# Optimization experiments

Measured on AMD Instinct MI355X. Metric: run time of the kernel, lower is better.

## Reference

```python
import jax, jax.numpy as jnp
import numpy as np

NUM_USERS = 100000
NUM_ITEMS = 50000
N_NODES = NUM_USERS + NUM_ITEMS
LATENT_DIM = 64
SBERT_DIM = 384
NUM_LAYERS = 3
N_EDGES = 2_000_000


def setup_inputs() -> dict:
    key = jax.random.key(0)
    k1, k2, k3, k4 = jax.random.split(key, 4)
    edge_index = jax.random.randint(k1, (2, N_EDGES), 0, N_NODES, dtype=jnp.int32)
    user_emb = jax.random.normal(k2, (NUM_USERS, LATENT_DIM), dtype=jnp.float32) * 0.1
    book_bert = jax.random.normal(k3, (NUM_ITEMS, SBERT_DIM), dtype=jnp.float32)
    # torch Linear weight layout: [out_features, in_features]
    w_proj = jax.random.normal(k4, (LATENT_DIM, SBERT_DIM), dtype=jnp.float32) * (1.0 / np.sqrt(SBERT_DIM))
    return {"edge_index": edge_index, "user_emb": user_emb, "book_bert": book_bert, "w_proj": w_proj}


def reference(edge_index, user_emb, book_bert, w_proj):
    src, dst = edge_index[0], edge_index[1]
    # initial embeddings: [users ; proj(book_bert)] -> [N, D]
    book_emb = book_bert @ w_proj.T
    emb0 = jnp.concatenate([user_emb, book_emb], axis=0)

    # symmetric gcn_norm without self-loops (PyG LGConv default)
    ones = jnp.ones((src.shape[0],), dtype=emb0.dtype)
    deg = jax.ops.segment_sum(ones, dst, num_segments=N_NODES)
    dis = jnp.where(deg > 0, jax.lax.rsqrt(jnp.maximum(deg, 1.0)), 0.0)
    norm = dis[src] * dis[dst]  # [E]

    x = emb0
    acc = emb0
    for _ in range(NUM_LAYERS):
        # out[dst] += norm * x[src]  (gather-scatter SpMM)
        msgs = norm[:, None] * x[src]  # [E, D]
        x = jax.ops.segment_sum(msgs, dst, num_segments=N_NODES)
        acc = acc + x
    out = acc / jnp.asarray(NUM_LAYERS + 1, dtype=emb0.dtype)
    return (emb0, out)
```

## Files before the change

kernel.cpp:

```cpp
#include <hip/hip_runtime.h>
#include <hip/hip_bf16.h>
#include <stdint.h>

#define NUM_USERS 100000
#define NUM_ITEMS 50000
#define N_NODES   150000
#define LATENT    64
#define SBERT     384
#define N_EDGES   2000000
#define OUT_OFF   (N_NODES * LATENT)
#define NBUCK     586
#define BCAP      4096
#define EPB       4096

typedef __hip_bfloat16 bf16;

__device__ __forceinline__ int ufl(int v) { return __builtin_amdgcn_readfirstlane(v); }

__global__ void k_zero_bcnt(int* __restrict__ bcnt) {
    int i = blockIdx.x * 256 + threadIdx.x;
    if (i < NBUCK) bcnt[i] = 0;
}

__global__ __launch_bounds__(256) void k_bin(const int* __restrict__ src,
                                             const int* __restrict__ dst,
                                             int* __restrict__ bcnt,
                                             unsigned* __restrict__ bin) {
    __shared__ int hist[NBUCK];
    __shared__ int base[NBUCK];
    const int tid = threadIdx.x;
    for (int i = tid; i < NBUCK; i += 256) hist[i] = 0;
    const int e0 = blockIdx.x * EPB;

    unsigned rec[16];
    int bb[16];
#pragma unroll
    for (int j = 0; j < 16; ++j) {
        int e = e0 + tid + j * 256;
        if (e < N_EDGES) {
            int d = __builtin_nontemporal_load(dst + e);
            int s = __builtin_nontemporal_load(src + e);
            bb[j]  = d >> 8;
            rec[j] = (unsigned)s | ((unsigned)(d & 255) << 18);
        } else {
            bb[j] = -1;
        }
    }
    __syncthreads();
#pragma unroll
    for (int j = 0; j < 16; ++j)
        if (bb[j] >= 0) atomicAdd(&hist[bb[j]], 1);
    __syncthreads();
    for (int i = tid; i < NBUCK; i += 256) {
        int c = hist[i];
        base[i] = c ? atomicAdd(&bcnt[i], c) : 0;
        hist[i] = 0;
    }
    __syncthreads();
    int p[16];
#pragma unroll
    for (int j = 0; j < 16; ++j)
        if (bb[j] >= 0) p[j] = atomicAdd(&hist[bb[j]], 1);
#pragma unroll
    for (int j = 0; j < 16; ++j)
        if (bb[j] >= 0)
            bin[(size_t)bb[j] * BCAP + base[bb[j]] + p[j]] = rec[j];
}

__global__ __launch_bounds__(1024) void k_bscan(const int* __restrict__ bcnt,
                                                int* __restrict__ bbase) {
    __shared__ int sm[1024];
    int tid = threadIdx.x;
    int v = (tid < NBUCK) ? bcnt[tid] : 0;
    sm[tid] = v;
    __syncthreads();
    for (int off = 1; off < 1024; off <<= 1) {
        int t = (tid >= off) ? sm[tid - off] : 0;
        __syncthreads();
        sm[tid] += t;
        __syncthreads();
    }
    if (tid <= NBUCK) bbase[tid] = (tid == 0) ? 0 : sm[tid - 1];
}

__global__ __launch_bounds__(256) void k_build(const unsigned* __restrict__ bin,
                                               const int* __restrict__ bcnt,
                                               const int* __restrict__ bbase,
                                               int* __restrict__ rp,
                                               float* __restrict__ dis,
                                               int* __restrict__ cws) {
    __shared__ int h[256];
    __shared__ int lc[256];
    const int tid   = threadIdx.x;
    const int b     = blockIdx.x;
    const int nbase = b << 8;
    const unsigned* mybin = bin + (size_t)b * BCAP;
    h[tid] = 0;
    __syncthreads();
    const int cnt  = bcnt[b];
    const int base = bbase[b];
    for (int i = tid; i < cnt; i += 256)
        atomicAdd(&h[__builtin_nontemporal_load(mybin + i) >> 18], 1);
    __syncthreads();
    int v = h[tid];
    __shared__ int sm[256];
    sm[tid] = v;
    __syncthreads();
    for (int off = 1; off < 256; off <<= 1) {
        int t = (tid >= off) ? sm[tid - off] : 0;
        __syncthreads();
        sm[tid] += t;
        __syncthreads();
    }
    int excl = sm[tid] - v;
    int n = nbase + tid;
    if (n < N_NODES) {
        rp[n]  = base + excl;
        dis[n] = (v > 0) ? rsqrtf((float)v) : 0.0f;
    }
    lc[tid] = base + excl;
    if (b == NBUCK - 1 && tid == 0) rp[N_NODES] = N_EDGES;
    __syncthreads();
    for (int i = tid; i < cnt; i += 256) {
        unsigned rec = __builtin_nontemporal_load(mybin + i);
        int dl = rec >> 18;
        int pos = atomicAdd(&lc[dl], 1);
        cws[pos] = (int)(rec & 0x3FFFF);
    }
}

__global__ void k_copy_user(const float* __restrict__ u, const float* __restrict__ dis,
                            float* __restrict__ out, bf16* __restrict__ y) {
    int i = blockIdx.x * 256 + threadIdx.x;
    if (i < NUM_USERS * LATENT) {
        float v = __builtin_nontemporal_load(u + i);
        out[i] = v;
        out[OUT_OFF + i] = v;
        float d = dis[i >> 6];
        y[i] = __float2bfloat16(d * v);
    }
}

__global__ __launch_bounds__(256) void k_proj(const float* __restrict__ bert,
                                              const float* __restrict__ w,
                                              const float* __restrict__ dis,
                                              float* __restrict__ out,
                                              bf16* __restrict__ y) {
    __shared__ float sB[128][33];
    __shared__ float sW[32][64];
    const int tid  = threadIdx.x;
    const int rb   = blockIdx.x * 128;
    const int col8 = (tid & 7) * 8;
    const int rowg = (tid >> 3) * 4;

    float acc[4][8];
#pragma unroll
    for (int i = 0; i < 4; ++i)
#pragma unroll
        for (int j = 0; j < 8; ++j) acc[i][j] = 0.0f;

    for (int kb = 0; kb < SBERT; kb += 32) {
        __syncthreads();
#pragma unroll
        for (int j = 0; j < 4; ++j) {
            int idx = tid + j * 256;
            int r  = idx >> 3;
            int k4 = (idx & 7) * 4;
            int rr = min(rb + r, NUM_ITEMS - 1);
            const float* bp = bert + (size_t)rr * SBERT + kb + k4;
            float4 v = make_float4(__builtin_nontemporal_load(bp + 0),
                                   __builtin_nontemporal_load(bp + 1),
                                   __builtin_nontemporal_load(bp + 2),
                                   __builtin_nontemporal_load(bp + 3));
            sB[r][k4 + 0] = v.x; sB[r][k4 + 1] = v.y;
            sB[r][k4 + 2] = v.z; sB[r][k4 + 3] = v.w;
        }
#pragma unroll
        for (int j = 0; j < 2; ++j) {
            int idx = tid + j * 256;
            int c  = idx >> 3;
            int k4 = (idx & 7) * 4;
            float4 v = *(const float4*)(w + (size_t)c * SBERT + kb + k4);
            sW[k4 + 0][c] = v.x; sW[k4 + 1][c] = v.y;
            sW[k4 + 2][c] = v.z; sW[k4 + 3][c] = v.w;
        }
        __syncthreads();
#pragma unroll
        for (int kk = 0; kk < 32; ++kk) {
            float4 w0 = *(const float4*)&sW[kk][col8];
            float4 w1 = *(const float4*)&sW[kk][col8 + 4];
#pragma unroll
            for (int i = 0; i < 4; ++i) {
                float a = sB[rowg + i][kk];
                acc[i][0] = fmaf(a, w0.x, acc[i][0]);
                acc[i][1] = fmaf(a, w0.y, acc[i][1]);
                acc[i][2] = fmaf(a, w0.z, acc[i][2]);
                acc[i][3] = fmaf(a, w0.w, acc[i][3]);
                acc[i][4] = fmaf(a, w1.x, acc[i][4]);
                acc[i][5] = fmaf(a, w1.y, acc[i][5]);
                acc[i][6] = fmaf(a, w1.z, acc[i][6]);
                acc[i][7] = fmaf(a, w1.w, acc[i][7]);
            }
        }
    }
#pragma unroll
    for (int i = 0; i < 4; ++i) {
        int r = rb + rowg + i;
        if (r < NUM_ITEMS) {
            int n = NUM_USERS + r;
            size_t o = (size_t)n * LATENT + col8;
            float d = dis[n];
            float4 f0 = make_float4(acc[i][0], acc[i][1], acc[i][2], acc[i][3]);
            float4 f1 = make_float4(acc[i][4], acc[i][5], acc[i][6], acc[i][7]);
            *(float4*)(out + o)           = f0;
            *(float4*)(out + o + 4)       = f1;
            *(float4*)(out + OUT_OFF + o) = f0;
            *(float4*)(out + OUT_OFF + o + 4) = f1;
#pragma unroll
            for (int j = 0; j < 8; ++j) y[o + j] = __float2bfloat16(d * acc[i][j]);
        }
    }
}

template <bool FINAL>
__global__ __launch_bounds__(256) void k_spmm(const bf16* __restrict__ y,
                                              const int* __restrict__ rp,
                                              const int* __restrict__ cws,
                                              const float* __restrict__ dis,
                                              bf16* __restrict__ yn,
                                              float* __restrict__ acc) {
    int lane = threadIdx.x & 63;
    int node = ufl(blockIdx.x * 4 + (threadIdx.x >> 6));
    int beg = rp[node];
    int end = rp[node + 1];
    int last = end - 1;
    float d = dis[node];
    size_t o = (size_t)node * LATENT + lane;
    float accv = acc[o];
    float a = 0.0f;
    for (int base = beg; base < end; base += 16) {
        int idx[16];
#pragma unroll
        for (int j = 0; j < 16; ++j)
            idx[j] = cws[min(base + j, last)];
        float v[16];
#pragma unroll
        for (int j = 0; j < 16; ++j)
            v[j] = __bfloat162float(y[(size_t)idx[j] * LATENT + lane]);
#pragma unroll
        for (int j = 0; j < 16; ++j)
            if (base + j <= last) a += v[j];
    }
    if (!FINAL) yn[o] = __float2bfloat16(d * d * a);
    float t = accv + d * a;
    acc[o] = FINAL ? t * 0.25f : t;
}

extern "C" void kernel_launch(void* const* d_in, const int* in_sizes, int n_in,
                              void* d_out, int out_size, void* d_ws, size_t ws_size,
                              hipStream_t stream) {
    const int*   ei    = (const int*)d_in[0];
    const float* uemb  = (const float*)d_in[1];
    const float* bert  = (const float*)d_in[2];
    const float* wproj = (const float*)d_in[3];
    float* out = (float*)d_out;

    char* ws = (char*)d_ws;
    size_t off = 0;
    auto carve = [&](size_t bytes) -> void* {
        void* p = ws + off;
        off += (bytes + 255) & ~(size_t)255;
        return p;
    };
    float*    dis    = (float*)carve(sizeof(float) * N_NODES);
    int*      rp     = (int*)carve(sizeof(int) * (N_NODES + 1));
    int*      bcnt   = (int*)carve(sizeof(int) * NBUCK);
    int*      bbase  = (int*)carve(sizeof(int) * (NBUCK + 1));
    unsigned* bin    = (unsigned*)carve(sizeof(unsigned) * (size_t)NBUCK * BCAP);
    int*      cws    = (int*)carve(sizeof(int) * N_EDGES);
    bf16*     ye     = (bf16*)carve(sizeof(bf16) * (size_t)N_NODES * LATENT);
    bf16*     y0     = (bf16*)carve(sizeof(bf16) * (size_t)N_NODES * LATENT);
    bf16*     y1     = (bf16*)carve(sizeof(bf16) * (size_t)N_NODES * LATENT);

    const int* srcI = ei;
    const int* dstI = ei + N_EDGES;

    k_zero_bcnt<<<(NBUCK + 255) / 256, 256, 0, stream>>>(bcnt);
    k_bin<<<(N_EDGES + EPB - 1) / EPB, 256, 0, stream>>>(srcI, dstI, bcnt, bin);
    k_bscan<<<1, 1024, 0, stream>>>(bcnt, bbase);
    k_build<<<NBUCK, 256, 0, stream>>>(bin, bcnt, bbase, rp, dis, cws);
    k_copy_user<<<(NUM_USERS * LATENT + 255) / 256, 256, 0, stream>>>(uemb, dis, out, ye);
    k_proj<<<(NUM_ITEMS + 127) / 128, 256, 0, stream>>>(bert, wproj, dis, out, ye);

    float* accp = out + OUT_OFF;
    k_spmm<false><<<N_NODES / 4, 256, 0, stream>>>(ye, rp, cws, dis, y0, accp);
    k_spmm<false><<<N_NODES / 4, 256, 0, stream>>>(y0, rp, cws, dis, y1, accp);
    k_spmm<true ><<<N_NODES / 4, 256, 0, stream>>>(y1, rp, cws, dis, y0, accp);
}
```

Baseline: 447.7 us.

## Fuse three SpMM layers into one cooperative persistent kernel with grid sync

```diff
diff --git a/kernel.cpp b/kernel.cpp
--- a/kernel.cpp
+++ b/kernel.cpp
@@ -1,6 +1,9 @@
 #include <hip/hip_runtime.h>
 #include <hip/hip_bf16.h>
+#include <hip/hip_cooperative_groups.h>
 #include <stdint.h>
+
+namespace cg = cooperative_groups;
 
 #define NUM_USERS 100000
 #define NUM_ITEMS 50000
@@ -12,6 +15,9 @@
 #define NBUCK     586
 #define BCAP      4096
 #define EPB       4096
+#define PBLK      1024
+#define PWAVES    4096
+#define NPW       37
 
 typedef __hip_bfloat16 bf16;
 
@@ -135,7 +141,6 @@
     if (i < NUM_USERS * LATENT) {
         float v = __builtin_nontemporal_load(u + i);
         out[i] = v;
-        out[OUT_OFF + i] = v;
         float d = dis[i >> 6];
         y[i] = __float2bfloat16(d * v);
     }
@@ -212,23 +217,85 @@
             float d = dis[n];
             float4 f0 = make_float4(acc[i][0], acc[i][1], acc[i][2], acc[i][3]);
             float4 f1 = make_float4(acc[i][4], acc[i][5], acc[i][6], acc[i][7]);
-            *(float4*)(out + o)           = f0;
-            *(float4*)(out + o + 4)       = f1;
-            *(float4*)(out + OUT_OFF + o) = f0;
-            *(float4*)(out + OUT_OFF + o + 4) = f1;
+            *(float4*)(out + o)     = f0;
+            *(float4*)(out + o + 4) = f1;
 #pragma unroll
             for (int j = 0; j < 8; ++j) y[o + j] = __float2bfloat16(d * acc[i][j]);
         }
     }
 }
 
-template <bool FINAL>
+__global__ __launch_bounds__(256, 4) void k_spmm3(const bf16* __restrict__ ye,
+                                                  bf16* __restrict__ y0,
+                                                  bf16* __restrict__ y1,
+                                                  const int* __restrict__ rp,
+                                                  const int* __restrict__ cws,
+                                                  const float* __restrict__ dis,
+                                                  float* __restrict__ out) {
+    cg::grid_group grid = cg::this_grid();
+    const int lane = threadIdx.x & 63;
+    const int w    = ufl(blockIdx.x * 4 + (threadIdx.x >> 6));
+
+    float acc[NPW];
+#pragma unroll
+    for (int k = 0; k < NPW; ++k) {
+        int node = w + (k << 12);
+        acc[k] = (node < N_NODES) ? out[(size_t)node * LATENT + lane] : 0.0f;
+    }
+
+    auto layer = [&](const bf16* __restrict__ ycur, bf16* __restrict__ ynext,
+                     bool final_) {
+#pragma unroll
+        for (int k = 0; k < NPW; ++k) {
+            int node = w + (k << 12);
+            if (node < N_NODES) {
+                int beg  = rp[node];
+                int end  = rp[node + 1];
+                int last = end - 1;
+                float d  = dis[node];
+                float a  = 0.0f;
+                for (int base = beg; base < end; base += 16) {
+                    int idx[16];
+#pragma unroll
+                    for (int j = 0; j < 16; ++j)
+                        idx[j] = cws[min(base + j, last)];
+                    float v[16];
+#pragma unroll
+                    for (int j = 0; j < 16; ++j)
+                        v[j] = __bfloat162float(ycur[(size_t)idx[j] * LATENT + lane]);
+#pragma unroll
+                    for (int j = 0; j < 16; ++j)
+                        if (base + j <= last) a += v[j];
+                }
+                acc[k] += d * a;
+                if (!final_)
+                    ynext[(size_t)node * LATENT + lane] = __float2bfloat16(d * d * a);
+            }
+        }
+    };
+
+    layer(ye, y0, false);
+    grid.sync();
+    layer(y0, y1, false);
+    grid.sync();
+    layer(y1, nullptr, true);
+
+#pragma unroll
+    for (int k = 0; k < NPW; ++k) {
+        int node = w + (k << 12);
+        if (node < N_NODES)
+            out[OUT_OFF + (size_t)node * LATENT + lane] = acc[k] * 0.25f;
+    }
+}
+
+template <bool FIRST, bool FINAL>
 __global__ __launch_bounds__(256) void k_spmm(const bf16* __restrict__ y,
                                               const int* __restrict__ rp,
                                               const int* __restrict__ cws,
                                               const float* __restrict__ dis,
                                               bf16* __restrict__ yn,
-                                              float* __restrict__ acc) {
+                                              float* __restrict__ acc,
+                                              const float* __restrict__ emb0) {
     int lane = threadIdx.x & 63;
     int node = ufl(blockIdx.x * 4 + (threadIdx.x >> 6));
     int beg = rp[node];
@@ -236,7 +303,7 @@
     int last = end - 1;
     float d = dis[node];
     size_t o = (size_t)node * LATENT + lane;
-    float accv = acc[o];
+    float accv = FIRST ? emb0[o] : acc[o];
     float a = 0.0f;
     for (int base = beg; base < end; base += 16) {
         int idx[16];
@@ -293,7 +360,28 @@
     k_proj<<<(NUM_ITEMS + 127) / 128, 256, 0, stream>>>(bert, wproj, dis, out, ye);
 
     float* accp = out + OUT_OFF;
-    k_spmm<false><<<N_NODES / 4, 256, 0, stream>>>(ye, rp, cws, dis, y0, accp);
-    k_spmm<false><<<N_NODES / 4, 256, 0, stream>>>(y0, rp, cws, dis, y1, accp);
-    k_spmm<true ><<<N_NODES / 4, 256, 0, stream>>>(y1, rp, cws, dis, y0, accp);
-}
+
+    static int coop_ok = -1;
+    if (coop_ok < 0) {
+        hipDeviceProp_t prop;
+        int dev = 0;
+        hipGetDevice(&dev);
+        hipGetDeviceProperties(&prop, dev);
+        int maxb = 0;
+        hipError_t e = hipOccupancyMaxActiveBlocksPerMultiprocessor(
+            &maxb, (const void*)k_spmm3, 256, 0);
+        coop_ok = (e == hipSuccess && prop.cooperativeLaunch &&
+                   maxb * prop.multiProcessorCount >= PBLK) ? 1 : 0;
+    }
+
+    if (coop_ok) {
+        void* args[] = {(void*)&ye, (void*)&y0, (void*)&y1, (void*)&rp,
+                        (void*)&cws, (void*)&dis, (void*)&out};
+        hipLaunchCooperativeKernel((void*)k_spmm3, dim3(PBLK), dim3(256),
+                                   args, 0, stream);
+    } else {
+        k_spmm<true,  false><<<N_NODES / 4, 256, 0, stream>>>(ye, rp, cws, dis, y0, accp, out);
+        k_spmm<false, false><<<N_NODES / 4, 256, 0, stream>>>(y0, rp, cws, dis, y1, accp, out);
+        k_spmm<false, true ><<<N_NODES / 4, 256, 0, stream>>>(y1, rp, cws, dis, y0, accp, out);
+    }
+}
```

After: 440.3 us. No clear change (-1.7%).
